# Optimization experiments

Measured on AMD Instinct MI355X. Metric: run time of the kernel, lower is better.

The kernel has to match this reference:

```python
import jax, jax.numpy as jnp
import numpy as np

N = 100000  # nodes
IN, HID, OUT = 64, 64, 32  # in_channels, 2*out_channels, out_channels
E = 1600000  # edges (avg degree 16)


def _gcn_conv(x, src, dst, deg_inv_sqrt, W, b, n):
    # PyG GCNConv: h = X W ; out[dst] += norm * h[src] ; out += b
    h = x @ W  # [N, F_out]
    norm = (deg_inv_sqrt[src] * deg_inv_sqrt[dst])[:, None]  # [E+N, 1]
    msg = h[src] * norm  # gathered edge messages [E+N, F_out]
    return jax.ops.segment_sum(msg, dst, num_segments=n) + b


def setup_inputs() -> dict:
    key = jax.random.key(0)
    ks = jax.random.split(key, 6)
    x = jax.random.normal(ks[0], (N, IN), dtype=jnp.float32)
    edge_index = jax.random.randint(ks[1], (2, E), 0, N, dtype=jnp.int32)
    # glorot-ish init for the two GCN layers
    W1 = jax.random.normal(ks[2], (IN, HID), dtype=jnp.float32) * (1.0 / np.sqrt(IN))
    b1 = jnp.zeros((HID,), dtype=jnp.float32)
    W2 = jax.random.normal(ks[3], (HID, OUT), dtype=jnp.float32) * (1.0 / np.sqrt(HID))
    b2 = jnp.zeros((OUT,), dtype=jnp.float32)
    return {"x": x, "edge_index": edge_index, "W1": W1, "b1": b1, "W2": W2, "b2": b2}


def reference(x, edge_index, W1, b1, W2, b2):
    n = x.shape[0]
    loop = jnp.arange(n, dtype=edge_index.dtype)
    src = jnp.concatenate([edge_index[0], loop])  # add self-loops
    dst = jnp.concatenate([edge_index[1], loop])
    # symmetric degree normalization (deg includes self-loops, so deg >= 1)
    deg = jax.ops.segment_sum(jnp.ones(dst.shape[0], x.dtype), dst, num_segments=n)
    dis = jax.lax.rsqrt(deg)
    h = jax.nn.relu(_gcn_conv(x, src, dst, dis, W1, b1, n))
    out = jax.nn.relu(_gcn_conv(h, src, dst, dis, W2, b2, n))
    return out
```

## Files before the change

### kernel.cpp

```cpp
#include <hip/hip_runtime.h>


#define NBMAX 512

__device__ __forceinline__ unsigned bf16pair(float a, float b) {
  unsigned ua = __float_as_uint(a), ub = __float_as_uint(b);
  ua = (ua + 0x7fffu + ((ua >> 16) & 1u)) >> 16;
  ub = (ub + 0x7fffu + ((ub >> 16) & 1u)) >> 16;
  return ua | (ub << 16);
}
__device__ __forceinline__ float bf_lo(unsigned v) { return __uint_as_float(v << 16); }
__device__ __forceinline__ float bf_hi(unsigned v) { return __uint_as_float(v & 0xffff0000u); }


__global__ __launch_bounds__(256) void k_coarsehist(const int* __restrict__ dst,
                                                    int* __restrict__ ch,
                                                    int E, int NB) {
  __shared__ int lh[NBMAX];
  int t = threadIdx.x;
  lh[t] = 0; lh[t + 256] = 0;
  __syncthreads();
  for (int e = blockIdx.x * 256 + t; e < E; e += gridDim.x * 256)
    atomicAdd(&lh[dst[e] >> 8], 1);
  __syncthreads();
  for (int b = t; b < NB; b += 256) {
    int c = lh[b];
    if (c) atomicAdd(&ch[b], c);
  }
}

__global__ __launch_bounds__(512) void k_scanb(const int* __restrict__ ch,
                                               int* __restrict__ cbase,
                                               int* __restrict__ gcur,
                                               int* __restrict__ off,
                                               int NB, int n, int E) {
  __shared__ int lds[512];
  int t = threadIdx.x;
  int v = (t < NB) ? ch[t] : 0;
  lds[t] = v;
  __syncthreads();
  for (int d = 1; d < 512; d <<= 1) {
    int u = (t >= d) ? lds[t - d] : 0;
    __syncthreads();
    lds[t] += u;
    __syncthreads();
  }
  if (t < NB) {
    int exc = lds[t] - v;
    cbase[t] = exc;
    gcur[t]  = exc;
  }
  if (t == 0) off[n] = E;
}

#define BIN_TILE 4096
__global__ __launch_bounds__(256) void k_binpairs(const int* __restrict__ src,
                                                  const int* __restrict__ dst,
                                                  int* __restrict__ gcur,
                                                  unsigned* __restrict__ pairs,
                                                  int E, int NB) {
  __shared__ int lcnt[NBMAX], gbase[NBMAX];
  int t = threadIdx.x;
  int tile0 = blockIdx.x * BIN_TILE;
  lcnt[t] = 0; lcnt[t + 256] = 0;
  __syncthreads();
#pragma unroll
  for (int j = 0; j < BIN_TILE / 256; ++j) {
    int e = tile0 + j * 256 + t;
    if (e < E) atomicAdd(&lcnt[dst[e] >> 8], 1);
  }
  __syncthreads();
  for (int b = t; b < NB; b += 256) {
    int c = lcnt[b];
    if (c) gbase[b] = atomicAdd(&gcur[b], c);
    lcnt[b] = 0;
  }
  __syncthreads();
#pragma unroll
  for (int j = 0; j < BIN_TILE / 256; ++j) {
    int e = tile0 + j * 256 + t;
    if (e < E) {
      int dv = dst[e];
      int b  = dv >> 8;
      int slot = atomicAdd(&lcnt[b], 1);
      pairs[gbase[b] + slot] = ((unsigned)src[e] << 8) | (unsigned)(dv & 255);
    }
  }
}

__global__ __launch_bounds__(512) void k_finesort(const unsigned* __restrict__ pairs,
                                                  const int* __restrict__ ch,
                                                  const int* __restrict__ cbase,
                                                  int* __restrict__ off,
                                                  float* __restrict__ dis,
                                                  int* __restrict__ ssrc, int n) {
  __shared__ int hist[256], lcur[256], wsum[4];
  __shared__ int sbuf[8192];
  int b = blockIdx.x;
  int node0 = b << 8;
  int nn = min(256, n - node0);
  int cnt = ch[b], base = cbase[b];
  int t = threadIdx.x;
  if (t < 256) hist[t] = 0;
  __syncthreads();
  for (int e = t; e < cnt; e += 512)
    atomicAdd(&hist[pairs[base + e] & 255u], 1);
  __syncthreads();
  int c = 0, inc = 0;
  if (t < 256) {
    c = hist[t];
    int lane = t & 63;
    inc = c;
#pragma unroll
    for (int d = 1; d < 64; d <<= 1) {
      int u = __shfl_up(inc, d);
      if (lane >= d) inc += u;
    }
    if (lane == 63) wsum[t >> 6] = inc;
  }
  __syncthreads();
  if (t < 256) {
    int wv = t >> 6;
    int pre = 0;
    for (int w = 0; w < wv; ++w) pre += wsum[w];
    int exc = pre + inc - c;
    if (t < nn) {
      off[node0 + t] = base + exc;
      dis[node0 + t] = rsqrtf((float)(c + 1));
    }
    lcur[t] = exc;
  }
  __syncthreads();
  bool inlds = (cnt <= 8192);
  for (int e = t; e < cnt; e += 512) {
    unsigned p = pairs[base + e];
    int slot = atomicAdd(&lcur[p & 255u], 1);
    int sv = (int)(p >> 8);
    if (inlds) sbuf[slot] = sv;
    else       ssrc[base + slot] = sv;
  }
  __syncthreads();
  if (inlds)
    for (int e = t; e < cnt; e += 512) ssrc[base + e] = sbuf[e];
}


__device__ __forceinline__ int swz(int r, int q) {
  return r * 16 + (q ^ ((r >> 3) & 7));
}

__global__ __launch_bounds__(128) void k_gemm64t(const float* __restrict__ X,
                                                 const float* __restrict__ W,
                                                 const float* __restrict__ dis,
                                                 unsigned* __restrict__ Hlo,
                                                 unsigned* __restrict__ Hhi, int n) {
  __shared__ float4 Xl[128 * 16];
  __shared__ float4 Wl[64 * 16];
  int t = threadIdx.x;
  int row0 = blockIdx.x * 128;
#pragma unroll
  for (int j = 0; j < 8; ++j) Wl[t + j * 128] = ((const float4*)W)[t + j * 128];
#pragma unroll
  for (int j = 0; j < 16; ++j) {
    int v = t + j * 128;
    int r = v >> 4, q = v & 15;
    int gr = row0 + r;
    float4 val = (gr < n) ? ((const float4*)X)[(size_t)gr * 16 + q]
                          : make_float4(0.f, 0.f, 0.f, 0.f);
    Xl[swz(r, q)] = val;
  }
  __syncthreads();
  int tx = t & 7, ty = t >> 3;
  float acc[8][8];
#pragma unroll
  for (int i = 0; i < 8; ++i)
#pragma unroll
    for (int j = 0; j < 8; ++j) acc[i][j] = 0.f;
  int tysw = ty & 7;
  for (int kq = 0; kq < 16; ++kq) {
    float x_[8][4];
#pragma unroll
    for (int i = 0; i < 8; ++i) {
      float4 v = Xl[(ty * 8 + i) * 16 + (kq ^ tysw)];
      x_[i][0] = v.x; x_[i][1] = v.y; x_[i][2] = v.z; x_[i][3] = v.w;
    }
#pragma unroll
    for (int kk = 0; kk < 4; ++kk) {
      int k = kq * 4 + kk;
      float4 w0 = Wl[k * 16 + tx * 2];
      float4 w1 = Wl[k * 16 + tx * 2 + 1];
      float w_[8] = {w0.x, w0.y, w0.z, w0.w, w1.x, w1.y, w1.z, w1.w};
#pragma unroll
      for (int i = 0; i < 8; ++i)
#pragma unroll
        for (int j = 0; j < 8; ++j)
          acc[i][j] = fmaf(x_[i][kk], w_[j], acc[i][j]);
    }
  }
  unsigned* Hb = (tx < 4) ? Hlo : Hhi;
  int txx = tx & 3;
#pragma unroll
  for (int i = 0; i < 8; ++i) {
    int r = row0 + ty * 8 + i;
    if (r < n) {
      float d = dis[r];
      uint4 o;
      o.x = bf16pair(acc[i][0] * d, acc[i][1] * d);
      o.y = bf16pair(acc[i][2] * d, acc[i][3] * d);
      o.z = bf16pair(acc[i][4] * d, acc[i][5] * d);
      o.w = bf16pair(acc[i][6] * d, acc[i][7] * d);
      ((uint4*)Hb)[(size_t)r * 4 + txx] = o;
    }
  }
}

__global__ __launch_bounds__(256) void k_gather64h(const int* __restrict__ off,
                                                   const int* __restrict__ ssrc,
                                                   const float* __restrict__ dis,
                                                   const uint2* __restrict__ Hb2,
                                                   const float* __restrict__ b1h,
                                                   float4* __restrict__ P4, int n) {
  int lane = threadIdx.x & 63;
  int q = lane & 7, g = lane >> 3;
  int i = blockIdx.x * 4 + (threadIdx.x >> 6);
  if (i >= n) return;
  int beg = off[i], end = off[i + 1];
  float s0 = 0.f, s1 = 0.f, s2 = 0.f, s3 = 0.f;
  if (g == 0) {
    uint2 v = Hb2[(size_t)i * 8 + q];
    s0 = bf_lo(v.x); s1 = bf_hi(v.x); s2 = bf_lo(v.y); s3 = bf_hi(v.y);
  }
  int e = beg + g;
  for (; e + 8 < end; e += 16) {
    uint2 v0 = Hb2[(size_t)ssrc[e]     * 8 + q];
    uint2 v1 = Hb2[(size_t)ssrc[e + 8] * 8 + q];
    s0 += bf_lo(v0.x) + bf_lo(v1.x);
    s1 += bf_hi(v0.x) + bf_hi(v1.x);
    s2 += bf_lo(v0.y) + bf_lo(v1.y);
    s3 += bf_hi(v0.y) + bf_hi(v1.y);
  }
  for (; e < end; e += 8) {
    uint2 v = Hb2[(size_t)ssrc[e] * 8 + q];
    s0 += bf_lo(v.x); s1 += bf_hi(v.x); s2 += bf_lo(v.y); s3 += bf_hi(v.y);
  }
  s0 += __shfl_xor(s0, 8);  s1 += __shfl_xor(s1, 8);
  s2 += __shfl_xor(s2, 8);  s3 += __shfl_xor(s3, 8);
  s0 += __shfl_xor(s0, 16); s1 += __shfl_xor(s1, 16);
  s2 += __shfl_xor(s2, 16); s3 += __shfl_xor(s3, 16);
  s0 += __shfl_xor(s0, 32); s1 += __shfl_xor(s1, 32);
  s2 += __shfl_xor(s2, 32); s3 += __shfl_xor(s3, 32);
  if (lane < 8) {
    float di = dis[i];
    float4 b = ((const float4*)b1h)[q];
    float4 o;
    o.x = fmaxf(fmaf(di, s0, b.x), 0.f);
    o.y = fmaxf(fmaf(di, s1, b.y), 0.f);
    o.z = fmaxf(fmaf(di, s2, b.z), 0.f);
    o.w = fmaxf(fmaf(di, s3, b.w), 0.f);
    P4[(size_t)i * 16 + q] = o;
  }
}


__global__ __launch_bounds__(128) void k_gemm32t(const float* __restrict__ P,
                                                 const float* __restrict__ W2,
                                                 const float* __restrict__ dis,
                                                 unsigned* __restrict__ Hb, int n) {
  __shared__ float4 Pl[128 * 16];
  __shared__ float4 Wl[64 * 8];
  int t = threadIdx.x;
  int row0 = blockIdx.x * 128;
#pragma unroll
  for (int j = 0; j < 4; ++j) Wl[t + j * 128] = ((const float4*)W2)[t + j * 128];
#pragma unroll
  for (int j = 0; j < 16; ++j) {
    int v = t + j * 128;
    int r = v >> 4, q = v & 15;
    int gr = row0 + r;
    float4 val = (gr < n) ? ((const float4*)P)[(size_t)gr * 16 + q]
                          : make_float4(0.f, 0.f, 0.f, 0.f);
    Pl[swz(r, q)] = val;
  }
  __syncthreads();
  int tx = t & 7, ty = t >> 3;
  float acc[8][4];
#pragma unroll
  for (int i = 0; i < 8; ++i)
#pragma unroll
    for (int j = 0; j < 4; ++j) acc[i][j] = 0.f;
  int tysw = ty & 7;
  for (int kq = 0; kq < 16; ++kq) {
    float x_[8][4];
#pragma unroll
    for (int i = 0; i < 8; ++i) {
      float4 v = Pl[(ty * 8 + i) * 16 + (kq ^ tysw)];
      x_[i][0] = v.x; x_[i][1] = v.y; x_[i][2] = v.z; x_[i][3] = v.w;
    }
#pragma unroll
    for (int kk = 0; kk < 4; ++kk) {
      int k = kq * 4 + kk;
      float4 w = Wl[k * 8 + tx];
      float w_[4] = {w.x, w.y, w.z, w.w};
#pragma unroll
      for (int i = 0; i < 8; ++i)
#pragma unroll
        for (int j = 0; j < 4; ++j)
          acc[i][j] = fmaf(x_[i][kk], w_[j], acc[i][j]);
    }
  }
#pragma unroll
  for (int i = 0; i < 8; ++i) {
    int r = row0 + ty * 8 + i;
    if (r < n) {
      float d = dis[r];
      uint2 o;
      o.x = bf16pair(acc[i][0] * d, acc[i][1] * d);
      o.y = bf16pair(acc[i][2] * d, acc[i][3] * d);
      ((uint2*)Hb)[(size_t)r * 8 + tx] = o;
    }
  }
}


__global__ __launch_bounds__(256) void k_gather32v(const int* __restrict__ off,
                                                   const int* __restrict__ ssrc,
                                                   const float* __restrict__ dis,
                                                   const uint2* __restrict__ Hb2,
                                                   const float* __restrict__ b2,
                                                   float* __restrict__ out, int n) {
  int lane = threadIdx.x & 63;
  int q = lane & 7, g = lane >> 3;
  int i = blockIdx.x * 4 + (threadIdx.x >> 6);
  if (i >= n) return;
  int beg = off[i], end = off[i + 1];
  float s0 = 0.f, s1 = 0.f, s2 = 0.f, s3 = 0.f;
  if (g == 0) {
    uint2 v = Hb2[(size_t)i * 8 + q];
    s0 = bf_lo(v.x); s1 = bf_hi(v.x); s2 = bf_lo(v.y); s3 = bf_hi(v.y);
  }
  int e = beg + g;
  for (; e + 8 < end; e += 16) {
    uint2 v0 = Hb2[(size_t)ssrc[e]     * 8 + q];
    uint2 v1 = Hb2[(size_t)ssrc[e + 8] * 8 + q];
    s0 += bf_lo(v0.x) + bf_lo(v1.x);
    s1 += bf_hi(v0.x) + bf_hi(v1.x);
    s2 += bf_lo(v0.y) + bf_lo(v1.y);
    s3 += bf_hi(v0.y) + bf_hi(v1.y);
  }
  for (; e < end; e += 8) {
    uint2 v = Hb2[(size_t)ssrc[e] * 8 + q];
    s0 += bf_lo(v.x); s1 += bf_hi(v.x); s2 += bf_lo(v.y); s3 += bf_hi(v.y);
  }
  s0 += __shfl_xor(s0, 8);  s1 += __shfl_xor(s1, 8);
  s2 += __shfl_xor(s2, 8);  s3 += __shfl_xor(s3, 8);
  s0 += __shfl_xor(s0, 16); s1 += __shfl_xor(s1, 16);
  s2 += __shfl_xor(s2, 16); s3 += __shfl_xor(s3, 16);
  s0 += __shfl_xor(s0, 32); s1 += __shfl_xor(s1, 32);
  s2 += __shfl_xor(s2, 32); s3 += __shfl_xor(s3, 32);
  if (lane < 8) {
    float di = dis[i];
    float4 b = ((const float4*)b2)[q];
    float4 o;
    o.x = fmaxf(fmaf(di, s0, b.x), 0.f);
    o.y = fmaxf(fmaf(di, s1, b.y), 0.f);
    o.z = fmaxf(fmaf(di, s2, b.z), 0.f);
    o.w = fmaxf(fmaf(di, s3, b.w), 0.f);
    ((float4*)out)[(size_t)i * 8 + q] = o;
  }
}

extern "C" void kernel_launch(void* const* d_in, const int* in_sizes, int n_in,
                              void* d_out, int out_size, void* d_ws, size_t ws_size,
                              hipStream_t stream) {
  const float* x  = (const float*)d_in[0];
  const int*   ei = (const int*)d_in[1];
  const float* W1 = (const float*)d_in[2];
  const float* b1 = (const float*)d_in[3];
  const float* W2 = (const float*)d_in[4];
  const float* b2 = (const float*)d_in[5];
  float* out = (float*)d_out;

  const int n = in_sizes[0] / 64;
  const int E = in_sizes[1] / 2;
  const int* src = ei;
  const int* dst = ei + E;
  const int NB = (n + 255) >> 8;

  char* wp = (char*)d_ws;
  auto alloc = [&](size_t bytes) {
    char* p = wp;
    wp += (bytes + 15) & ~(size_t)15;
    return (void*)p;
  };
  unsigned* pairs = (unsigned*)alloc((size_t)E * 4);
  int*      ch    = (int*)alloc(NBMAX * 4);
  int*      cbase = (int*)alloc(NBMAX * 4);
  int*      gcur  = (int*)alloc(NBMAX * 4);
  int*      off   = (int*)alloc(((size_t)n + 1) * 4);
  float*    dis   = (float*)alloc((size_t)n * 4);
  int*      ssrc  = (int*)alloc((size_t)E * 4);
  unsigned* h1lo  = (unsigned*)alloc((size_t)n * 32 * 2);
  unsigned* h1hi  = (unsigned*)alloc((size_t)n * 32 * 2);
  float*    p1    = (float*)alloc((size_t)n * 64 * 4);
  unsigned* h2b   = (unsigned*)alloc((size_t)n * 32 * 2);

  auto cdiv = [](long long a, long long b) { return (unsigned)((a + b - 1) / b); };
  dim3 B(256);

  hipMemsetAsync(ch, 0, (size_t)NBMAX * 4, stream);
  k_coarsehist<<<512, B, 0, stream>>>(dst, ch, E, NB);
  k_scanb     <<<1, 512, 0, stream>>>(ch, cbase, gcur, off, NB, n, E);
  k_binpairs  <<<cdiv(E, BIN_TILE), B, 0, stream>>>(src, dst, gcur, pairs, E, NB);
  k_finesort  <<<NB, 512, 0, stream>>>(pairs, ch, cbase, off, dis, ssrc, n);

  k_gemm64t   <<<cdiv(n, 128), 128, 0, stream>>>(x, W1, dis, h1lo, h1hi, n);
  k_gather64h <<<cdiv(n, 4), B, 0, stream>>>(off, ssrc, dis, (const uint2*)h1lo,
                                             b1,      (float4*)p1,     n);
  k_gather64h <<<cdiv(n, 4), B, 0, stream>>>(off, ssrc, dis, (const uint2*)h1hi,
                                             b1 + 32, (float4*)p1 + 8, n);
  k_gemm32t   <<<cdiv(n, 128), 128, 0, stream>>>(p1, W2, dis, h2b, n);
  k_gather32v <<<cdiv(n, 4), B, 0, stream>>>(off, ssrc, dis, (const uint2*)h2b, b2, out, n);
}
```

Measured before the change: 224.1 us.

## Merge split-half layer-1 gather into one full-width pass with nontemporal hints

The first-layer features are now stored as one contiguous 64-wide bf16 row instead of two 32-wide halves. A single gather kernel aggregates all 64 channels, using 16 lanes per edge and 4 edge groups, where before two launches each walked the CSR index list. This halves the ssrc/offset traffic and removes one launch, but the per-row random gather becomes 128 bytes and each lane group covers fewer edges in parallel. Index loads and output stores also use nontemporal hints to reduce cache pollution.

```diff
diff --git a/kernel.cpp b/kernel.cpp
--- a/kernel.cpp
+++ b/kernel.cpp
@@ -2,6 +2,9 @@
 
 
 #define NBMAX 512
+#define BIN_TILE 4096
+
+typedef float f32x4 __attribute__((ext_vector_type(4)));
 
 __device__ __forceinline__ unsigned bf16pair(float a, float b) {
   unsigned ua = __float_as_uint(a), ub = __float_as_uint(b);
@@ -53,7 +56,6 @@
   if (t == 0) off[n] = E;
 }
 
-#define BIN_TILE 4096
 __global__ __launch_bounds__(256) void k_binpairs(const int* __restrict__ src,
                                                   const int* __restrict__ dst,
                                                   int* __restrict__ gcur,
@@ -152,8 +154,7 @@
 __global__ __launch_bounds__(128) void k_gemm64t(const float* __restrict__ X,
                                                  const float* __restrict__ W,
                                                  const float* __restrict__ dis,
-                                                 unsigned* __restrict__ Hlo,
-                                                 unsigned* __restrict__ Hhi, int n) {
+                                                 unsigned* __restrict__ Hb, int n) {
   __shared__ float4 Xl[128 * 16];
   __shared__ float4 Wl[64 * 16];
   int t = threadIdx.x;
@@ -197,8 +198,6 @@
           acc[i][j] = fmaf(x_[i][kk], w_[j], acc[i][j]);
     }
   }
-  unsigned* Hb = (tx < 4) ? Hlo : Hhi;
-  int txx = tx & 3;
 #pragma unroll
   for (int i = 0; i < 8; ++i) {
     int r = row0 + ty * 8 + i;
@@ -209,17 +208,125 @@
       o.y = bf16pair(acc[i][2] * d, acc[i][3] * d);
       o.z = bf16pair(acc[i][4] * d, acc[i][5] * d);
       o.w = bf16pair(acc[i][6] * d, acc[i][7] * d);
-      ((uint4*)Hb)[(size_t)r * 4 + txx] = o;
-    }
-  }
-}
-
-__global__ __launch_bounds__(256) void k_gather64h(const int* __restrict__ off,
+      ((uint4*)Hb)[(size_t)r * 8 + tx] = o;
+    }
+  }
+}
+
+__global__ __launch_bounds__(128) void k_gemm32t(const float* __restrict__ P,
+                                                 const float* __restrict__ W2,
+                                                 const float* __restrict__ dis,
+                                                 unsigned* __restrict__ Hb, int n) {
+  __shared__ float4 Pl[128 * 16];
+  __shared__ float4 Wl[64 * 8];
+  int t = threadIdx.x;
+  int row0 = blockIdx.x * 128;
+#pragma unroll
+  for (int j = 0; j < 4; ++j) Wl[t + j * 128] = ((const float4*)W2)[t + j * 128];
+#pragma unroll
+  for (int j = 0; j < 16; ++j) {
+    int v = t + j * 128;
+    int r = v >> 4, q = v & 15;
+    int gr = row0 + r;
+    float4 val = (gr < n) ? ((const float4*)P)[(size_t)gr * 16 + q]
+                          : make_float4(0.f, 0.f, 0.f, 0.f);
+    Pl[swz(r, q)] = val;
+  }
+  __syncthreads();
+  int tx = t & 7, ty = t >> 3;
+  float acc[8][4];
+#pragma unroll
+  for (int i = 0; i < 8; ++i)
+#pragma unroll
+    for (int j = 0; j < 4; ++j) acc[i][j] = 0.f;
+  int tysw = ty & 7;
+  for (int kq = 0; kq < 16; ++kq) {
+    float x_[8][4];
+#pragma unroll
+    for (int i = 0; i < 8; ++i) {
+      float4 v = Pl[(ty * 8 + i) * 16 + (kq ^ tysw)];
+      x_[i][0] = v.x; x_[i][1] = v.y; x_[i][2] = v.z; x_[i][3] = v.w;
+    }
+#pragma unroll
+    for (int kk = 0; kk < 4; ++kk) {
+      int k = kq * 4 + kk;
+      float4 w = Wl[k * 8 + tx];
+      float w_[4] = {w.x, w.y, w.z, w.w};
+#pragma unroll
+      for (int i = 0; i < 8; ++i)
+#pragma unroll
+        for (int j = 0; j < 4; ++j)
+          acc[i][j] = fmaf(x_[i][kk], w_[j], acc[i][j]);
+    }
+  }
+#pragma unroll
+  for (int i = 0; i < 8; ++i) {
+    int r = row0 + ty * 8 + i;
+    if (r < n) {
+      float d = dis[r];
+      uint2 o;
+      o.x = bf16pair(acc[i][0] * d, acc[i][1] * d);
+      o.y = bf16pair(acc[i][2] * d, acc[i][3] * d);
+      ((uint2*)Hb)[(size_t)r * 8 + tx] = o;
+    }
+  }
+}
+
+
+__global__ __launch_bounds__(256) void k_gather64v(const int* __restrict__ off,
                                                    const int* __restrict__ ssrc,
                                                    const float* __restrict__ dis,
                                                    const uint2* __restrict__ Hb2,
-                                                   const float* __restrict__ b1h,
-                                                   float4* __restrict__ P4, int n) {
+                                                   const float* __restrict__ b1,
+                                                   f32x4* __restrict__ P4, int n) {
+  int lane = threadIdx.x & 63;
+  int q = lane & 15, g = lane >> 4;
+  int i = blockIdx.x * 4 + (threadIdx.x >> 6);
+  if (i >= n) return;
+  int beg = off[i], end = off[i + 1];
+  float s0 = 0.f, s1 = 0.f, s2 = 0.f, s3 = 0.f;
+  if (g == 0) {
+    uint2 v = Hb2[(size_t)i * 16 + q];
+    s0 = bf_lo(v.x); s1 = bf_hi(v.x); s2 = bf_lo(v.y); s3 = bf_hi(v.y);
+  }
+  int e = beg + g;
+  for (; e + 4 < end; e += 8) {
+    int i0 = __builtin_nontemporal_load(&ssrc[e]);
+    int i1 = __builtin_nontemporal_load(&ssrc[e + 4]);
+    uint2 v0 = Hb2[(size_t)i0 * 16 + q];
+    uint2 v1 = Hb2[(size_t)i1 * 16 + q];
+    s0 += bf_lo(v0.x) + bf_lo(v1.x);
+    s1 += bf_hi(v0.x) + bf_hi(v1.x);
+    s2 += bf_lo(v0.y) + bf_lo(v1.y);
+    s3 += bf_hi(v0.y) + bf_hi(v1.y);
+  }
+  for (; e < end; e += 4) {
+    int i0 = __builtin_nontemporal_load(&ssrc[e]);
+    uint2 v = Hb2[(size_t)i0 * 16 + q];
+    s0 += bf_lo(v.x); s1 += bf_hi(v.x); s2 += bf_lo(v.y); s3 += bf_hi(v.y);
+  }
+  s0 += __shfl_xor(s0, 16); s1 += __shfl_xor(s1, 16);
+  s2 += __shfl_xor(s2, 16); s3 += __shfl_xor(s3, 16);
+  s0 += __shfl_xor(s0, 32); s1 += __shfl_xor(s1, 32);
+  s2 += __shfl_xor(s2, 32); s3 += __shfl_xor(s3, 32);
+  if (lane < 16) {
+    float di = dis[i];
+    float4 b = ((const float4*)b1)[q];
+    f32x4 o;
+    o.x = fmaxf(fmaf(di, s0, b.x), 0.f);
+    o.y = fmaxf(fmaf(di, s1, b.y), 0.f);
+    o.z = fmaxf(fmaf(di, s2, b.z), 0.f);
+    o.w = fmaxf(fmaf(di, s3, b.w), 0.f);
+    __builtin_nontemporal_store(o, &P4[(size_t)i * 16 + q]);
+  }
+}
+
+__global__ __launch_bounds__(256) void k_gather32v(const int* __restrict__ off,
+                                                   const int* __restrict__ ssrc,
+                                                   const float* __restrict__ dis,
+                                                   const uint2* __restrict__ Hb2,
+                                                   const float* __restrict__ b2,
+                                                   f32x4* __restrict__ out4, int n) {
   int lane = threadIdx.x & 63;
   int q = lane & 7, g = lane >> 3;
   int i = blockIdx.x * 4 + (threadIdx.x >> 6);
@@ -232,123 +339,18 @@
   }
   int e = beg + g;
   for (; e + 8 < end; e += 16) {
-    uint2 v0 = Hb2[(size_t)ssrc[e]     * 8 + q];
-    uint2 v1 = Hb2[(size_t)ssrc[e + 8] * 8 + q];
+    int i0 = __builtin_nontemporal_load(&ssrc[e]);
+    int i1 = __builtin_nontemporal_load(&ssrc[e + 8]);
+    uint2 v0 = Hb2[(size_t)i0 * 8 + q];
+    uint2 v1 = Hb2[(size_t)i1 * 8 + q];
     s0 += bf_lo(v0.x) + bf_lo(v1.x);
     s1 += bf_hi(v0.x) + bf_hi(v1.x);
     s2 += bf_lo(v0.y) + bf_lo(v1.y);
     s3 += bf_hi(v0.y) + bf_hi(v1.y);
   }
   for (; e < end; e += 8) {
-    uint2 v = Hb2[(size_t)ssrc[e] * 8 + q];
-    s0 += bf_lo(v.x); s1 += bf_hi(v.x); s2 += bf_lo(v.y); s3 += bf_hi(v.y);
-  }
-  s0 += __shfl_xor(s0, 8);  s1 += __shfl_xor(s1, 8);
-  s2 += __shfl_xor(s2, 8);  s3 += __shfl_xor(s3, 8);
-  s0 += __shfl_xor(s0, 16); s1 += __shfl_xor(s1, 16);
-  s2 += __shfl_xor(s2, 16); s3 += __shfl_xor(s3, 16);
-  s0 += __shfl_xor(s0, 32); s1 += __shfl_xor(s1, 32);
-  s2 += __shfl_xor(s2, 32); s3 += __shfl_xor(s3, 32);
-  if (lane < 8) {
-    float di = dis[i];
-    float4 b = ((const float4*)b1h)[q];
-    float4 o;
-    o.x = fmaxf(fmaf(di, s0, b.x), 0.f);
-    o.y = fmaxf(fmaf(di, s1, b.y), 0.f);
-    o.z = fmaxf(fmaf(di, s2, b.z), 0.f);
-    o.w = fmaxf(fmaf(di, s3, b.w), 0.f);
-    P4[(size_t)i * 16 + q] = o;
-  }
-}
-
-
-__global__ __launch_bounds__(128) void k_gemm32t(const float* __restrict__ P,
-                                                 const float* __restrict__ W2,
-                                                 const float* __restrict__ dis,
-                                                 unsigned* __restrict__ Hb, int n) {
-  __shared__ float4 Pl[128 * 16];
-  __shared__ float4 Wl[64 * 8];
-  int t = threadIdx.x;
-  int row0 = blockIdx.x * 128;
-#pragma unroll
-  for (int j = 0; j < 4; ++j) Wl[t + j * 128] = ((const float4*)W2)[t + j * 128];
-#pragma unroll
-  for (int j = 0; j < 16; ++j) {
-    int v = t + j * 128;
-    int r = v >> 4, q = v & 15;
-    int gr = row0 + r;
-    float4 val = (gr < n) ? ((const float4*)P)[(size_t)gr * 16 + q]
-                          : make_float4(0.f, 0.f, 0.f, 0.f);
-    Pl[swz(r, q)] = val;
-  }
-  __syncthreads();
-  int tx = t & 7, ty = t >> 3;
-  float acc[8][4];
-#pragma unroll
-  for (int i = 0; i < 8; ++i)
-#pragma unroll
-    for (int j = 0; j < 4; ++j) acc[i][j] = 0.f;
-  int tysw = ty & 7;
-  for (int kq = 0; kq < 16; ++kq) {
-    float x_[8][4];
-#pragma unroll
-    for (int i = 0; i < 8; ++i) {
-      float4 v = Pl[(ty * 8 + i) * 16 + (kq ^ tysw)];
-      x_[i][0] = v.x; x_[i][1] = v.y; x_[i][2] = v.z; x_[i][3] = v.w;
-    }
-#pragma unroll
-    for (int kk = 0; kk < 4; ++kk) {
-      int k = kq * 4 + kk;
-      float4 w = Wl[k * 8 + tx];
-      float w_[4] = {w.x, w.y, w.z, w.w};
-#pragma unroll
-      for (int i = 0; i < 8; ++i)
-#pragma unroll
-        for (int j = 0; j < 4; ++j)
-          acc[i][j] = fmaf(x_[i][kk], w_[j], acc[i][j]);
-    }
-  }
-#pragma unroll
-  for (int i = 0; i < 8; ++i) {
-    int r = row0 + ty * 8 + i;
-    if (r < n) {
-      float d = dis[r];
-      uint2 o;
-      o.x = bf16pair(acc[i][0] * d, acc[i][1] * d);
-      o.y = bf16pair(acc[i][2] * d, acc[i][3] * d);
-      ((uint2*)Hb)[(size_t)r * 8 + tx] = o;
-    }
-  }
-}
-
-
-__global__ __launch_bounds__(256) void k_gather32v(const int* __restrict__ off,
-                                                   const int* __restrict__ ssrc,
-                                                   const float* __restrict__ dis,
-                                                   const uint2* __restrict__ Hb2,
-                                                   const float* __restrict__ b2,
-                                                   float* __restrict__ out, int n) {
-  int lane = threadIdx.x & 63;
-  int q = lane & 7, g = lane >> 3;
-  int i = blockIdx.x * 4 + (threadIdx.x >> 6);
-  if (i >= n) return;
-  int beg = off[i], end = off[i + 1];
-  float s0 = 0.f, s1 = 0.f, s2 = 0.f, s3 = 0.f;
-  if (g == 0) {
-    uint2 v = Hb2[(size_t)i * 8 + q];
-    s0 = bf_lo(v.x); s1 = bf_hi(v.x); s2 = bf_lo(v.y); s3 = bf_hi(v.y);
-  }
-  int e = beg + g;
-  for (; e + 8 < end; e += 16) {
-    uint2 v0 = Hb2[(size_t)ssrc[e]     * 8 + q];
-    uint2 v1 = Hb2[(size_t)ssrc[e + 8] * 8 + q];
-    s0 += bf_lo(v0.x) + bf_lo(v1.x);
-    s1 += bf_hi(v0.x) + bf_hi(v1.x);
-    s2 += bf_lo(v0.y) + bf_lo(v1.y);
-    s3 += bf_hi(v0.y) + bf_hi(v1.y);
-  }
-  for (; e < end; e += 8) {
-    uint2 v = Hb2[(size_t)ssrc[e] * 8 + q];
+    int i0 = __builtin_nontemporal_load(&ssrc[e]);
+    uint2 v = Hb2[(size_t)i0 * 8 + q];
     s0 += bf_lo(v.x); s1 += bf_hi(v.x); s2 += bf_lo(v.y); s3 += bf_hi(v.y);
   }
   s0 += __shfl_xor(s0, 8);  s1 += __shfl_xor(s1, 8);
@@ -360,12 +362,12 @@
   if (lane < 8) {
     float di = dis[i];
     float4 b = ((const float4*)b2)[q];
-    float4 o;
+    f32x4 o;
     o.x = fmaxf(fmaf(di, s0, b.x), 0.f);
     o.y = fmaxf(fmaf(di, s1, b.y), 0.f);
     o.z = fmaxf(fmaf(di, s2, b.z), 0.f);
     o.w = fmaxf(fmaf(di, s3, b.w), 0.f);
-    ((float4*)out)[(size_t)i * 8 + q] = o;
+    __builtin_nontemporal_store(o, &out4[(size_t)i * 8 + q]);
   }
 }
 
@@ -399,25 +401,23 @@
   int*      off   = (int*)alloc(((size_t)n + 1) * 4);
   float*    dis   = (float*)alloc((size_t)n * 4);
   int*      ssrc  = (int*)alloc((size_t)E * 4);
-  unsigned* h1lo  = (unsigned*)alloc((size_t)n * 32 * 2);
-  unsigned* h1hi  = (unsigned*)alloc((size_t)n * 32 * 2);
+  unsigned* h1b   = (unsigned*)alloc((size_t)n * 64 * 2);
   float*    p1    = (float*)alloc((size_t)n * 64 * 4);
   unsigned* h2b   = (unsigned*)alloc((size_t)n * 32 * 2);
 
   auto cdiv = [](long long a, long long b) { return (unsigned)((a + b - 1) / b); };
   dim3 B(256);
 
-  hipMemsetAsync(ch, 0, (size_t)NBMAX * 4, stream);
+  (void)hipMemsetAsync(ch, 0, (size_t)NBMAX * 4, stream);
   k_coarsehist<<<512, B, 0, stream>>>(dst, ch, E, NB);
   k_scanb     <<<1, 512, 0, stream>>>(ch, cbase, gcur, off, NB, n, E);
   k_binpairs  <<<cdiv(E, BIN_TILE), B, 0, stream>>>(src, dst, gcur, pairs, E, NB);
   k_finesort  <<<NB, 512, 0, stream>>>(pairs, ch, cbase, off, dis, ssrc, n);
 
-  k_gemm64t   <<<cdiv(n, 128), 128, 0, stream>>>(x, W1, dis, h1lo, h1hi, n);
-  k_gather64h <<<cdiv(n, 4), B, 0, stream>>>(off, ssrc, dis, (const uint2*)h1lo,
-                                             b1,      (float4*)p1,     n);
-  k_gather64h <<<cdiv(n, 4), B, 0, stream>>>(off, ssrc, dis, (const uint2*)h1hi,
-                                             b1 + 32, (float4*)p1 + 8, n);
+  k_gemm64t   <<<cdiv(n, 128), 128, 0, stream>>>(x, W1, dis, h1b, n);
+  k_gather64v <<<cdiv(n, 4), B, 0, stream>>>(off, ssrc, dis, (const uint2*)h1b, b1,
+                                             (f32x4*)p1, n);
   k_gemm32t   <<<cdiv(n, 128), 128, 0, stream>>>(p1, W2, dis, h2b, n);
-  k_gather32v <<<cdiv(n, 4), B, 0, stream>>>(off, ssrc, dis, (const uint2*)h2b, b2, out, n);
-}
+  k_gather32v <<<cdiv(n, 4), B, 0, stream>>>(off, ssrc, dis, (const uint2*)h2b, b2,
+                                             (f32x4*)out, n);
+}
```

Result: faster. 216.0 us (-3.6%).
